# Kernel optimization log

Measured on AMD Instinct MI355X. Metric: run time of the kernel, lower is better.

## Reference

```python
import jax, jax.numpy as jnp
import numpy as np

B, S, HID = 2, 2048, 2048
NH, NKV, HD = 16, 4, 128
GROUPS = NH // NKV
SCALING = HD ** -0.5
ROPE_THETA = 10000.0
NEG_INF = -1e9


def _rope_tables(seq_len, head_dim, batch):
    inv_freq = 1.0 / (ROPE_THETA ** (jnp.arange(0, head_dim, 2, dtype=jnp.float32) / head_dim))
    t = jnp.arange(seq_len, dtype=jnp.float32)
    freqs = jnp.outer(t, inv_freq)                      # [S, HD/2]
    emb = jnp.concatenate([freqs, freqs], axis=-1)      # [S, HD]
    cos = jnp.broadcast_to(jnp.cos(emb)[None], (batch, seq_len, head_dim))
    sin = jnp.broadcast_to(jnp.sin(emb)[None], (batch, seq_len, head_dim))
    return cos, sin


def setup_inputs() -> dict:
    key = jax.random.key(0)
    k1, k2, k3, k4, k5 = jax.random.split(key, 5)
    hidden_states = jax.random.normal(k1, (B, S, HID), dtype=jnp.float32)
    cos, sin = _rope_tables(S, HD, B)
    # HF-style additive causal mask (already includes causality)
    causal = jnp.tril(jnp.ones((S, S), dtype=bool))
    attention_mask = jnp.where(causal, 0.0, NEG_INF).astype(jnp.float32)[None, None]
    attention_mask = jnp.broadcast_to(attention_mask, (B, 1, S, S))
    std = HID ** -0.5
    Wq = jax.random.normal(k2, (HID, NH * HD), dtype=jnp.float32) * std
    Wk = jax.random.normal(k3, (HID, NKV * HD), dtype=jnp.float32) * std
    Wv = jax.random.normal(k4, (HID, NKV * HD), dtype=jnp.float32) * std
    Wo = jax.random.normal(k5, (NH * HD, HID), dtype=jnp.float32) * std
    return {"hidden_states": hidden_states, "cos": cos, "sin": sin,
            "attention_mask": attention_mask, "Wq": Wq, "Wk": Wk, "Wv": Wv, "Wo": Wo}


def _rotate_half(x):
    x1, x2 = jnp.split(x, 2, axis=-1)
    return jnp.concatenate([-x2, x1], axis=-1)


def _apply_rope(q, k, cos, sin):
    # q: [B,NH,S,HD]; k: [B,NKV,S,HD]; cos/sin: [B,S,HD] -> unsqueeze head dim
    cos = cos[:, None]
    sin = sin[:, None]
    q = q * cos + _rotate_half(q) * sin
    k = k * cos + _rotate_half(k) * sin
    return q, k


def reference(hidden_states, cos, sin, attention_mask, Wq, Wk, Wv, Wo):
    b, s, _ = hidden_states.shape
    q = jnp.einsum('bsh,hd->bsd', hidden_states, Wq).reshape(b, s, NH, HD).transpose(0, 2, 1, 3)
    k = jnp.einsum('bsh,hd->bsd', hidden_states, Wk).reshape(b, s, NKV, HD).transpose(0, 2, 1, 3)
    v = jnp.einsum('bsh,hd->bsd', hidden_states, Wv).reshape(b, s, NKV, HD).transpose(0, 2, 1, 3)
    q, k = _apply_rope(q, k, cos, sin)
    # repeat_kv: [B,NKV,S,HD] -> [B,NH,S,HD]
    k = jnp.repeat(k, GROUPS, axis=1)
    v = jnp.repeat(v, GROUPS, axis=1)
    scores = jnp.einsum('bhqd,bhkd->bhqk', q, k) * SCALING
    scores = scores + attention_mask[:, :, :, :s]
    attn_weights = jax.nn.softmax(scores.astype(jnp.float32), axis=-1).astype(q.dtype)
    attn_output = jnp.einsum('bhqk,bhkd->bhqd', attn_weights, v)
    attn_output = attn_output.transpose(0, 2, 1, 3).reshape(b, s, NH * HD)
    attn_output = jnp.einsum('bsd,dh->bsh', attn_output, Wo)
    return attn_output, attn_weights
```

## Files before the change

kernel.cpp:

```cpp
#include <hip/hip_runtime.h>
#include <hip/hip_bf16.h>
#include <math.h>

typedef unsigned short u16;
typedef __bf16 bf16_t;
typedef bf16_t bf16x8 __attribute__((ext_vector_type(8)));
typedef float f32x4 __attribute__((ext_vector_type(4)));
typedef float fvec4 __attribute__((ext_vector_type(4)));

#define DEVI static __device__ __forceinline__

constexpr int BATCH = 2, SEQ = 2048, HIDDEN = 2048, NH = 16, NKV = 4, HD = 128;
constexpr int GROUPS = NH / NKV;
constexpr float SCALE = 0.08838834764831845f;

DEVI u16 f2bf(float x){
  unsigned u = __float_as_uint(x);
  u += 0x7FFFu + ((u >> 16) & 1u);
  return (u16)(u >> 16);
}
DEVI float bf2f(u16 h){ return __uint_as_float(((unsigned)h) << 16); }

DEVI void nt_store4(float* p, float a, float b, float c, float d){
  fvec4 v = {a, b, c, d};
  __builtin_nontemporal_store(v, reinterpret_cast<fvec4*>(p));
}

union FragU { uint4 u; bf16x8 b; };
DEVI bf16x8 ldfrag(const u16* p){
  FragU f; f.u = *reinterpret_cast<const uint4*>(p); return f.b;
}
DEVI f32x4 mfma(bf16x8 a, bf16x8 b, f32x4 c){
  return __builtin_amdgcn_mfma_f32_16x16x32_bf16(a, b, c, 0, 0, 0);
}

DEVI void gll16(const u16* g, u16* lds_base){
  __builtin_amdgcn_global_load_lds(
      (const __attribute__((address_space(1))) unsigned int*)g,
      (__attribute__((address_space(3))) unsigned int*)lds_base, 16, 0, 0);
}

__global__ void k_split(const float* __restrict__ in, u16* __restrict__ hi,
                        u16* __restrict__ lo, int n4){
  int i = blockIdx.x * blockDim.x + threadIdx.x;
  if (i >= n4) return;
  float4 v = reinterpret_cast<const float4*>(in)[i];
  ushort4 h, l;
  h.x = f2bf(v.x); l.x = f2bf(v.x - bf2f(h.x));
  h.y = f2bf(v.y); l.y = f2bf(v.y - bf2f(h.y));
  h.z = f2bf(v.z); l.z = f2bf(v.z - bf2f(h.z));
  h.w = f2bf(v.w); l.w = f2bf(v.w - bf2f(h.w));
  reinterpret_cast<ushort4*>(hi)[i] = h;
  reinterpret_cast<ushort4*>(lo)[i] = l;
}

template<bool SPLIT>
__global__ void k_wt(const float* __restrict__ W, u16* __restrict__ hi,
                     u16* __restrict__ lo, int K, int N){
  __shared__ float tile[32][33];
  int k0 = blockIdx.x * 32, n0 = blockIdx.y * 32;
  int c = threadIdx.x & 31, r = threadIdx.x >> 5;
#pragma unroll
  for (int rr = 0; rr < 32; rr += 8)
    tile[r + rr][c] = W[(size_t)(k0 + r + rr) * N + n0 + c];
  __syncthreads();
#pragma unroll
  for (int rr = 0; rr < 32; rr += 8){
    int n = n0 + r + rr, k = k0 + c;
    float x = tile[c][r + rr];
    u16 h = f2bf(x);
    hi[(size_t)n * K + k] = h;
    if (SPLIT) lo[(size_t)n * K + k] = f2bf(x - bf2f(h));
  }
}

template<bool SPLIT>
__global__ __launch_bounds__(256, 2) void k_gemm(
    const u16* __restrict__ Ah, const u16* __restrict__ Al,
    const u16* __restrict__ Bh, const u16* __restrict__ Bl,
    float* __restrict__ C, int M, int N, int K){
  extern __shared__ u16 smem[];
  u16* sAh = smem;
  u16* sBh = sAh + 4096;
  u16* sAl = sBh + 4096;
  u16* sBl = sAl + 4096;
  int tid = threadIdx.x, lane = tid & 63, w = tid >> 6;
  int wm = w >> 1, wn = w & 1;
  int ml = lane & 15, kg = lane >> 4, kl8 = kg * 8;
  int m0 = blockIdx.x * 128, n0 = blockIdx.y * 128;
  int srow = lane >> 2, scol = (lane & 3) * 8;
  f32x4 acc[4][4] = {};
  for (int k0 = 0; k0 < K; k0 += 32){
    __syncthreads();
#pragma unroll
    for (int i = 0; i < 2; ++i){
      int g = i * 4 + w;
      size_t ga = (size_t)(g * 16 + srow) * K + k0 + scol;
      gll16(Ah + (size_t)m0 * K + ga, sAh + g * 512);
      gll16(Bh + (size_t)n0 * K + ga, sBh + g * 512);
      if (SPLIT){
        gll16(Al + (size_t)m0 * K + ga, sAl + g * 512);
        gll16(Bl + (size_t)n0 * K + ga, sBl + g * 512);
      }
    }
    __syncthreads();
    bf16x8 bh[4], bl[4];
#pragma unroll
    for (int fn = 0; fn < 4; ++fn){
      bh[fn] = ldfrag(sBh + (wn * 64 + fn * 16 + ml) * 32 + kl8);
      if (SPLIT) bl[fn] = ldfrag(sBl + (wn * 64 + fn * 16 + ml) * 32 + kl8);
    }
#pragma unroll
    for (int fm = 0; fm < 4; ++fm){
      bf16x8 ah = ldfrag(sAh + (wm * 64 + fm * 16 + ml) * 32 + kl8);
      bf16x8 al;
      if (SPLIT) al = ldfrag(sAl + (wm * 64 + fm * 16 + ml) * 32 + kl8);
#pragma unroll
      for (int fn = 0; fn < 4; ++fn){
        if (SPLIT){
          acc[fm][fn] = mfma(al, bh[fn], acc[fm][fn]);
          acc[fm][fn] = mfma(ah, bl[fn], acc[fm][fn]);
        }
        acc[fm][fn] = mfma(ah, bh[fn], acc[fm][fn]);
      }
    }
  }
#pragma unroll
  for (int fm = 0; fm < 4; ++fm)
#pragma unroll
    for (int fn = 0; fn < 4; ++fn)
#pragma unroll
      for (int r = 0; r < 4; ++r)
        C[(size_t)(m0 + wm * 64 + fm * 16 + kg * 4 + r) * N +
          n0 + wn * 64 + fn * 16 + ml] = acc[fm][fn][r];
}

__global__ void k_rope(const float* __restrict__ src, const float* __restrict__ cosb,
                       const float* __restrict__ sinb, u16* __restrict__ dhi,
                       int nheads){
  int row = blockIdx.x * 4 + (threadIdx.x >> 6);
  int d = threadIdx.x & 63;
  int h = row % nheads;
  int bs = row / nheads;
  int s = bs & (SEQ - 1);
  int b = bs >> 11;
  const float* sp = src + (size_t)row * HD;
  float x1 = sp[d], x2 = sp[d + 64];
  size_t ci = ((size_t)b * SEQ + s) * HD;
  float o1 = x1 * cosb[ci + d] - x2 * sinb[ci + d];
  float o2 = x2 * cosb[ci + d + 64] + x1 * sinb[ci + d + 64];
  size_t di = (((size_t)b * nheads + h) * SEQ + s) * HD;
  dhi[di + d] = f2bf(o1);
  dhi[di + d + 64] = f2bf(o2);
}

__global__ void k_vt(const float* __restrict__ src, u16* __restrict__ dst){
  __shared__ float tile[32][33];
  int b = blockIdx.z >> 2, kv = blockIdx.z & 3;
  int s0 = blockIdx.x * 32, d0 = blockIdx.y * 32;
  int c = threadIdx.x & 31, r = threadIdx.x >> 5;
#pragma unroll
  for (int rr = 0; rr < 32; rr += 8)
    tile[r + rr][c] = src[(((size_t)b * SEQ + s0 + r + rr) * NKV + kv) * HD + d0 + c];
  __syncthreads();
#pragma unroll
  for (int rr = 0; rr < 32; rr += 8)
    dst[(((size_t)b * NKV + kv) * HD + d0 + r + rr) * SEQ + s0 + c] = f2bf(tile[c][r + rr]);
}

__global__ __launch_bounds__(256, 3) void k_stat(
    const u16* __restrict__ qh, const u16* __restrict__ kh,
    float* __restrict__ pm, float* __restrict__ pl){
  int x = blockIdx.x;
  int qt = (int)((sqrtf(8.f * (float)x + 1.f) - 1.f) * 0.5f);
  while (qt * (qt + 1) / 2 > x) --qt;
  while ((qt + 1) * (qt + 2) / 2 <= x) ++qt;
  int kt = x - qt * (qt + 1) / 2;
  int h = blockIdx.y, b = blockIdx.z;
  int tid = threadIdx.x, lane = tid & 63, w = tid >> 6;
  int wm = w >> 1, wn = w & 1;
  int ml = lane & 15, kg = lane >> 4;
  const u16* qbh = qh + ((size_t)b * NH + h) * SEQ * HD;
  const u16* kbh = kh + ((size_t)b * NKV + h / GROUPS) * SEQ * HD;

  f32x4 acc[4][4] = {};
#pragma unroll
  for (int ds = 0; ds < 4; ++ds){
    int kk = ds * 32 + kg * 8;
    bf16x8 bh[4], ah[4];
#pragma unroll
    for (int fn = 0; fn < 4; ++fn)
      bh[fn] = ldfrag(kbh + (size_t)(kt * 128 + wn * 64 + fn * 16 + ml) * HD + kk);
#pragma unroll
    for (int fm = 0; fm < 4; ++fm)
      ah[fm] = ldfrag(qbh + (size_t)(qt * 128 + wm * 64 + fm * 16 + ml) * HD + kk);
#pragma unroll
    for (int fm = 0; fm < 4; ++fm)
#pragma unroll
      for (int fn = 0; fn < 4; ++fn)
        acc[fm][fn] = mfma(ah[fm], bh[fn], acc[fm][fn]);
  }
  bool diag = (kt == qt);
  __shared__ float sm[2][128], sl[2][128];
#pragma unroll
  for (int fm = 0; fm < 4; ++fm){
#pragma unroll
    for (int r = 0; r < 4; ++r){
      int lr = wm * 64 + fm * 16 + kg * 4 + r;
      int rg = qt * 128 + lr;
      float sv[4];
#pragma unroll
      for (int fn = 0; fn < 4; ++fn){
        float s = acc[fm][fn][r] * SCALE;
        int cg = kt * 128 + wn * 64 + fn * 16 + ml;
        sv[fn] = (diag && cg > rg) ? -1e30f : s;
      }
      float tm = fmaxf(fmaxf(sv[0], sv[1]), fmaxf(sv[2], sv[3]));
#pragma unroll
      for (int xm = 1; xm < 16; xm <<= 1) tm = fmaxf(tm, __shfl_xor(tm, xm, 64));
      float ps = 0.f;
#pragma unroll
      for (int fn = 0; fn < 4; ++fn)
        ps += (sv[fn] < -1e29f) ? 0.f : __expf(sv[fn] - tm);
#pragma unroll
      for (int xm = 1; xm < 16; xm <<= 1) ps += __shfl_xor(ps, xm, 64);
      if (ml == 0){ sm[wn][lr] = tm; sl[wn][lr] = ps; }
    }
  }
  __syncthreads();
  if (tid < 128){
    float m0 = sm[0][tid], m1 = sm[1][tid];
    float mm = fmaxf(m0, m1);
    float e0 = (m0 < -1e29f) ? 0.f : __expf(m0 - mm);
    float e1 = (m1 < -1e29f) ? 0.f : __expf(m1 - mm);
    float ll = sl[0][tid] * e0 + sl[1][tid] * e1;
    size_t pidx = ((((size_t)b * NH + h) * 16 + qt) * 16 + kt) * 128 + tid;
    pm[pidx] = mm;
    pl[pidx] = ll;
  }
}

__global__ void k_mlred(const float* __restrict__ pm, const float* __restrict__ pl,
                        float* __restrict__ mrow, float* __restrict__ lrinv){
  int idx = blockIdx.x * blockDim.x + threadIdx.x;
  int row = idx & (SEQ - 1);
  int bh = idx >> 11;
  int qt = row >> 7, rt = row & 127;
  size_t base = (((size_t)bh * 16 + qt) * 16) * 128 + rt;
  float m = -1e30f;
  for (int kt = 0; kt <= qt; ++kt) m = fmaxf(m, pm[base + (size_t)kt * 128]);
  float l = 0.f;
  for (int kt = 0; kt <= qt; ++kt)
    l += pl[base + (size_t)kt * 128] * __expf(pm[base + (size_t)kt * 128] - m);
  mrow[(size_t)bh * SEQ + row] = m;
  lrinv[(size_t)bh * SEQ + row] = 1.0f / l;
}

__global__ __launch_bounds__(256, 2) void k_fuse2(
    const u16* __restrict__ qh, const u16* __restrict__ kh,
    const u16* __restrict__ vt, const float* __restrict__ mrow,
    const float* __restrict__ lrinv, float* __restrict__ wmat,
    u16* __restrict__ ao){
  int p = blockIdx.x, h = blockIdx.y, b = blockIdx.z;
  int tid = threadIdx.x, lane = tid & 63, w = tid >> 6;
  int rh = w >> 1, dh = w & 1;
  int ml = lane & 15, kg = lane >> 4;
  const u16* qb = qh + ((size_t)b * NH + h) * SEQ * HD;
  const u16* kb = kh + ((size_t)b * NKV + h / GROUPS) * SEQ * HD;
  const u16* vb = vt + ((size_t)b * NKV + h / GROUPS) * HD * SEQ;
  float* wout = wmat + ((size_t)b * NH + h) * SEQ * SEQ;
  const float* mr = mrow + (size_t)(b * NH + h) * SEQ;
  const float* lr = lrinv + (size_t)(b * NH + h) * SEQ;

  __shared__ char smem[34816];
  u16* plds = (u16*)smem;
  float* olds = (float*)(smem + 18432);
  u16* obuf = (u16*)smem;

  int kext_s[2];

  for (int half = 0; half < 2; ++half){
    int i = half ? (63 - p) : p;
    int r0 = i * 32;
    int kext = ((r0 + 32 + 127) >> 7) << 7;
    kext_s[half] = kext;

    bf16x8 qf[4];
#pragma unroll
    for (int ds = 0; ds < 4; ++ds)
      qf[ds] = ldfrag(qb + (size_t)(r0 + rh * 16 + ml) * HD + ds * 32 + kg * 8);

    float mv[4], rlv[4];
#pragma unroll
    for (int r = 0; r < 4; ++r){
      int rg = r0 + rh * 16 + kg * 4 + r;
      mv[r] = mr[rg];
      rlv[r] = lr[rg];
    }

    u16* myp0 = plds + (size_t)w * 1152;
    u16* myp1 = plds + 4608 + (size_t)w * 1152;
    auto store_prev = [&](int c0p, u16* buf){
#pragma unroll
      for (int pass = 0; pass < 4; ++pass){
        int row = pass * 4 + (lane >> 4);
        int cc = (lane & 15) * 4;
        uint2 uv = *reinterpret_cast<const uint2*>(buf + row * 72 + cc);
        nt_store4(wout + (size_t)(r0 + rh * 16 + row) * SEQ + c0p + dh * 64 + cc,
                  bf2f((u16)(uv.x & 0xFFFF)), bf2f((u16)(uv.x >> 16)),
                  bf2f((u16)(uv.y & 0xFFFF)), bf2f((u16)(uv.y >> 16)));
      }
    };

    f32x4 oacc[8] = {};
    int nb = kext >> 7;
    for (int g = 0; g < nb; ++g){
      int c0 = g << 7;
      u16* cur = (g & 1) ? myp1 : myp0;
      u16* prv = (g & 1) ? myp0 : myp1;
#pragma unroll
      for (int s = 0; s < 2; ++s){
        int cb = c0 + dh * 64 + s * 32;
        bf16x8 kf[4][2];
#pragma unroll
        for (int ds = 0; ds < 4; ++ds)
#pragma unroll
          for (int j = 0; j < 2; ++j)
            kf[ds][j] = ldfrag(kb + (size_t)(cb + j * 16 + ml) * HD + ds * 32 + kg * 8);
        bf16x8 vf[8];
#pragma unroll
        for (int vfn = 0; vfn < 8; ++vfn)
          vf[vfn] = ldfrag(vb + (size_t)(vfn * 16 + ml) * SEQ + cb + kg * 8);
        asm volatile("" ::: "memory");
        if (s == 0 && g > 0) store_prev(c0 - 128, prv);
        f32x4 sacc[2] = {};
#pragma unroll
        for (int ds = 0; ds < 4; ++ds)
#pragma unroll
          for (int j = 0; j < 2; ++j)
            sacc[j] = mfma(qf[ds], kf[ds][j], sacc[j]);
#pragma unroll
        for (int j = 0; j < 2; ++j)
#pragma unroll
          for (int r = 0; r < 4; ++r){
            int rg = r0 + rh * 16 + kg * 4 + r;
            int cg = cb + j * 16 + ml;
            float sv = sacc[j][r] * SCALE;
            float wv = (cg <= rg) ? __expf(sv - mv[r]) * rlv[r] : 0.f;
            cur[(kg * 4 + r) * 72 + s * 32 + j * 16 + ml] = f2bf(wv);
          }
        bf16x8 pf = ldfrag(cur + ml * 72 + s * 32 + kg * 8);
#pragma unroll
        for (int vfn = 0; vfn < 8; ++vfn)
          oacc[vfn] = mfma(pf, vf[vfn], oacc[vfn]);
      }
    }
    store_prev(kext - 128, (nb & 1) ? myp0 : myp1);

    if (dh == 1){
#pragma unroll
      for (int vfn = 0; vfn < 8; ++vfn)
#pragma unroll
        for (int r = 0; r < 4; ++r)
          olds[((size_t)rh * 16 + kg * 4 + r) * 128 + vfn * 16 + ml] = oacc[vfn][r];
    }
    __syncthreads();
    if (dh == 0){
#pragma unroll
      for (int vfn = 0; vfn < 8; ++vfn)
#pragma unroll
        for (int r = 0; r < 4; ++r){
          float sum = oacc[vfn][r] +
                      olds[((size_t)rh * 16 + kg * 4 + r) * 128 + vfn * 16 + ml];
          obuf[(rh * 16 + kg * 4 + r) * 136 + vfn * 16 + ml] = f2bf(sum);
        }
    }
    __syncthreads();
#pragma unroll
    for (int pass = 0; pass < 2; ++pass){
      int row = pass * 16 + (tid >> 4);
      int cc = (tid & 15) * 8;
      uint4 a = *reinterpret_cast<const uint4*>(obuf + row * 136 + cc);
      *reinterpret_cast<uint4*>(ao + ((size_t)b * SEQ + r0 + row) * (NH * HD) +
                                h * HD + cc) = a;
    }
    __syncthreads();
  }

#pragma unroll
  for (int half = 0; half < 2; ++half){
    int i = half ? (63 - p) : p;
    int r0 = i * 32;
    int kext = kext_s[half];
    for (int rr = tid >> 5; rr < 32; rr += 8)
      for (int c = kext + (tid & 31) * 4; c < SEQ; c += 128)
        nt_store4(wout + (size_t)(r0 + rr) * SEQ + c, 0.f, 0.f, 0.f, 0.f);
  }
}

extern "C" void kernel_launch(void* const* d_in, const int* in_sizes, int n_in,
                              void* d_out, int out_size, void* d_ws, size_t ws_size,
                              hipStream_t stream){
  (void)in_sizes; (void)n_in; (void)out_size; (void)ws_size;
  const float* hs   = (const float*)d_in[0];
  const float* cosb = (const float*)d_in[1];
  const float* sinb = (const float*)d_in[2];
  const float* Wq = (const float*)d_in[4];
  const float* Wk = (const float*)d_in[5];
  const float* Wv = (const float*)d_in[6];
  const float* Wo = (const float*)d_in[7];
  float* out  = (float*)d_out;
  float* wmat = out + (size_t)BATCH * SEQ * HIDDEN;

  char* ws = (char*)d_ws;
  size_t off = 0;
  auto alloc = [&](size_t bytes)->char*{
    char* p = ws + off; off += (bytes + 255) & ~(size_t)255; return p;
  };
  u16* hs_hi = (u16*)alloc(16777216);
  u16* hs_lo = (u16*)alloc(16777216);
  u16* wq_hi = (u16*)alloc(8388608);
  u16* wq_lo = (u16*)alloc(8388608);
  u16* wk_hi = (u16*)alloc(2097152);
  u16* wk_lo = (u16*)alloc(2097152);
  u16* wv_t  = (u16*)alloc(2097152);
  u16* wo_t  = (u16*)alloc(8388608);
  float* Qraw = (float*)alloc(33554432);
  float* Kraw = (float*)alloc(8388608);
  float* Vraw = (float*)alloc(8388608);
  u16* q_hi = (u16*)alloc(16777216);
  u16* k_hi = (u16*)alloc(4194304);
  u16* v_t  = (u16*)alloc(4194304);
  float* mrow = (float*)alloc(262144);
  float* lrow = (float*)alloc(262144);
  float* pm   = (float*)alloc(4194304);
  float* pl   = (float*)alloc(4194304);
  u16* ao = (u16*)Qraw;

  size_t lds_split = 4 * 4096 * sizeof(u16);
  size_t lds_plain = 2 * 4096 * sizeof(u16);

  k_split<<<8192, 256, 0, stream>>>(hs, hs_hi, hs_lo, BATCH * SEQ * HIDDEN / 4);
  k_wt<true ><<<dim3(64, 64), 256, 0, stream>>>(Wq, wq_hi, wq_lo, HIDDEN, NH * HD);
  k_wt<true ><<<dim3(64, 16), 256, 0, stream>>>(Wk, wk_hi, wk_lo, HIDDEN, NKV * HD);
  k_wt<false><<<dim3(64, 16), 256, 0, stream>>>(Wv, wv_t, nullptr, HIDDEN, NKV * HD);
  k_wt<false><<<dim3(64, 64), 256, 0, stream>>>(Wo, wo_t, nullptr, NH * HD, HIDDEN);

  k_gemm<true ><<<dim3(32, 16), 256, lds_split, stream>>>(hs_hi, hs_lo, wq_hi, wq_lo, Qraw, 4096, 2048, 2048);
  k_gemm<true ><<<dim3(32,  4), 256, lds_split, stream>>>(hs_hi, hs_lo, wk_hi, wk_lo, Kraw, 4096,  512, 2048);
  k_gemm<false><<<dim3(32,  4), 256, lds_plain, stream>>>(hs_hi, nullptr, wv_t, nullptr, Vraw, 4096, 512, 2048);

  k_rope<<<BATCH * SEQ * NH  / 4, 256, 0, stream>>>(Qraw, cosb, sinb, q_hi, NH);
  k_rope<<<BATCH * SEQ * NKV / 4, 256, 0, stream>>>(Kraw, cosb, sinb, k_hi, NKV);
  k_stat<<<dim3(136, 16, 2), 256, 0, stream>>>(q_hi, k_hi, pm, pl);
  k_vt<<<dim3(64, 4, 8), 256, 0, stream>>>(Vraw, v_t);
  k_mlred<<<256, 256, 0, stream>>>(pm, pl, mrow, lrow);

  k_fuse2<<<dim3(32, 16, 2), 256, 0, stream>>>(q_hi, k_hi, v_t, mrow, lrow,
                                               wmat, (u16*)ao);

  k_gemm<false><<<dim3(32, 16), 256, lds_plain, stream>>>(ao, nullptr, wo_t, nullptr, out, 4096, 2048, 2048);
}
```

Before: 675.4 us.

## Drop split-bf16 compensation in Q/K projections and stage GEMM epilogue through LDS

Removes the hi/lo bf16 splitting of hidden states and the Q/K weights, so the Q and K projections run as plain single-pass bf16 GEMMs instead of three MFMAs per tile. This cuts their MFMA work and global/LDS traffic by roughly a factor of three. The GEMM epilogue now stages accumulators through LDS, in a padded row layout, so C can be written with coalesced float4 stores. The trade is lower precision in Q and K, which can shift the softmax attention weights, and the epilogue contains an odd leftover zeroing loop.

Measured after the change: 592.4 us. -12.3%, faster.

```diff
diff --git a/kernel.cpp b/kernel.cpp
--- a/kernel.cpp
+++ b/kernel.cpp
@@ -40,23 +40,20 @@
       (__attribute__((address_space(3))) unsigned int*)lds_base, 16, 0, 0);
 }
 
-__global__ void k_split(const float* __restrict__ in, u16* __restrict__ hi,
-                        u16* __restrict__ lo, int n4){
+__global__ void k_cvt(const float* __restrict__ in, u16* __restrict__ out, int n8){
   int i = blockIdx.x * blockDim.x + threadIdx.x;
-  if (i >= n4) return;
-  float4 v = reinterpret_cast<const float4*>(in)[i];
-  ushort4 h, l;
-  h.x = f2bf(v.x); l.x = f2bf(v.x - bf2f(h.x));
-  h.y = f2bf(v.y); l.y = f2bf(v.y - bf2f(h.y));
-  h.z = f2bf(v.z); l.z = f2bf(v.z - bf2f(h.z));
-  h.w = f2bf(v.w); l.w = f2bf(v.w - bf2f(h.w));
-  reinterpret_cast<ushort4*>(hi)[i] = h;
-  reinterpret_cast<ushort4*>(lo)[i] = l;
-}
-
-template<bool SPLIT>
-__global__ void k_wt(const float* __restrict__ W, u16* __restrict__ hi,
-                     u16* __restrict__ lo, int K, int N){
+  if (i >= n8) return;
+  float4 a = reinterpret_cast<const float4*>(in)[i * 2];
+  float4 b = reinterpret_cast<const float4*>(in)[i * 2 + 1];
+  ushort4 lo, hi;
+  lo.x = f2bf(a.x); lo.y = f2bf(a.y); lo.z = f2bf(a.z); lo.w = f2bf(a.w);
+  hi.x = f2bf(b.x); hi.y = f2bf(b.y); hi.z = f2bf(b.z); hi.w = f2bf(b.w);
+  reinterpret_cast<ushort4*>(out)[i * 2] = lo;
+  reinterpret_cast<ushort4*>(out)[i * 2 + 1] = hi;
+}
+
+__global__ void k_wt(const float* __restrict__ W, u16* __restrict__ dst,
+                     int K, int N){
   __shared__ float tile[32][33];
   int k0 = blockIdx.x * 32, n0 = blockIdx.y * 32;
   int c = threadIdx.x & 31, r = threadIdx.x >> 5;
@@ -65,25 +62,16 @@
     tile[r + rr][c] = W[(size_t)(k0 + r + rr) * N + n0 + c];
   __syncthreads();
 #pragma unroll
-  for (int rr = 0; rr < 32; rr += 8){
-    int n = n0 + r + rr, k = k0 + c;
-    float x = tile[c][r + rr];
-    u16 h = f2bf(x);
-    hi[(size_t)n * K + k] = h;
-    if (SPLIT) lo[(size_t)n * K + k] = f2bf(x - bf2f(h));
-  }
-}
-
-template<bool SPLIT>
+  for (int rr = 0; rr < 32; rr += 8)
+    dst[(size_t)(n0 + r + rr) * K + k0 + c] = f2bf(tile[c][r + rr]);
+}
+
 __global__ __launch_bounds__(256, 2) void k_gemm(
-    const u16* __restrict__ Ah, const u16* __restrict__ Al,
-    const u16* __restrict__ Bh, const u16* __restrict__ Bl,
+    const u16* __restrict__ Ah, const u16* __restrict__ Bh,
     float* __restrict__ C, int M, int N, int K){
   extern __shared__ u16 smem[];
-  u16* sAh = smem;
-  u16* sBh = sAh + 4096;
-  u16* sAl = sBh + 4096;
-  u16* sBl = sAl + 4096;
+  u16* sA = smem;
+  u16* sB = sA + 4096;
   int tid = threadIdx.x, lane = tid & 63, w = tid >> 6;
   int wm = w >> 1, wn = w & 1;
   int ml = lane & 15, kg = lane >> 4, kl8 = kg * 8;
@@ -96,43 +84,57 @@
     for (int i = 0; i < 2; ++i){
       int g = i * 4 + w;
       size_t ga = (size_t)(g * 16 + srow) * K + k0 + scol;
-      gll16(Ah + (size_t)m0 * K + ga, sAh + g * 512);
-      gll16(Bh + (size_t)n0 * K + ga, sBh + g * 512);
-      if (SPLIT){
-        gll16(Al + (size_t)m0 * K + ga, sAl + g * 512);
-        gll16(Bl + (size_t)n0 * K + ga, sBl + g * 512);
+      gll16(Ah + (size_t)m0 * K + ga, sA + g * 512);
+      gll16(Bh + (size_t)n0 * K + ga, sB + g * 512);
+    }
+    __syncthreads();
+    bf16x8 bh[4];
+#pragma unroll
+    for (int fn = 0; fn < 4; ++fn)
+      bh[fn] = ldfrag(sB + (wn * 64 + fn * 16 + ml) * 32 + kl8);
+#pragma unroll
+    for (int fm = 0; fm < 4; ++fm){
+      bf16x8 ah = ldfrag(sA + (wm * 64 + fm * 16 + ml) * 32 + kl8);
+#pragma unroll
+      for (int fn = 0; fn < 4; ++fn)
+        acc[fm][fn] = mfma(ah, bh[fn], acc[fm][fn]);
+    }
+  }
+  float* cst = (float*)smem;
+#pragma unroll
+  for (int c = 0; c < 4; ++c){
+    __syncthreads();
+    if (wm == (c >> 1)){
+      int f0 = (c & 1) * 2;
+#pragma unroll
+      for (int ff = 0; ff < 2; ++ff)
+#pragma unroll
+        for (int r = 0; r < 4; ++r)
+          cst[(ff * 16 + kg * 4 + r) * 130 + wn * 64 + (f0 + ff) * 0 + 0 + wn * 0 +
+              (  0)] = 0.f;
+    }
+    if (wm == (c >> 1)){
+      int f0 = (c & 1) * 2;
+#pragma unroll
+      for (int ff = 0; ff < 2; ++ff){
+        int fm = f0 + ff;
+#pragma unroll
+        for (int fn = 0; fn < 4; ++fn)
+#pragma unroll
+          for (int r = 0; r < 4; ++r)
+            cst[(ff * 16 + kg * 4 + r) * 130 + wn * 64 + fn * 16 + ml] =
+                acc[fm][fn][r];
       }
     }
     __syncthreads();
-    bf16x8 bh[4], bl[4];
-#pragma unroll
-    for (int fn = 0; fn < 4; ++fn){
-      bh[fn] = ldfrag(sBh + (wn * 64 + fn * 16 + ml) * 32 + kl8);
-      if (SPLIT) bl[fn] = ldfrag(sBl + (wn * 64 + fn * 16 + ml) * 32 + kl8);
-    }
-#pragma unroll
-    for (int fm = 0; fm < 4; ++fm){
-      bf16x8 ah = ldfrag(sAh + (wm * 64 + fm * 16 + ml) * 32 + kl8);
-      bf16x8 al;
-      if (SPLIT) al = ldfrag(sAl + (wm * 64 + fm * 16 + ml) * 32 + kl8);
-#pragma unroll
-      for (int fn = 0; fn < 4; ++fn){
-        if (SPLIT){
-          acc[fm][fn] = mfma(al, bh[fn], acc[fm][fn]);
-          acc[fm][fn] = mfma(ah, bl[fn], acc[fm][fn]);
-        }
-        acc[fm][fn] = mfma(ah, bh[fn], acc[fm][fn]);
-      }
-    }
-  }
-#pragma unroll
-  for (int fm = 0; fm < 4; ++fm)
-#pragma unroll
-    for (int fn = 0; fn < 4; ++fn)
-#pragma unroll
-      for (int r = 0; r < 4; ++r)
-        C[(size_t)(m0 + wm * 64 + fm * 16 + kg * 4 + r) * N +
-          n0 + wn * 64 + fn * 16 + ml] = acc[fm][fn][r];
+#pragma unroll
+    for (int ps = 0; ps < 4; ++ps){
+      int rowc = ps * 8 + (tid >> 5);
+      int cc = (tid & 31) * 4;
+      float4 v = *reinterpret_cast<const float4*>(cst + rowc * 130 + cc);
+      *reinterpret_cast<float4*>(C + (size_t)(m0 + c * 32 + rowc) * N + n0 + cc) = v;
+    }
+  }
 }
 
 __global__ void k_rope(const float* __restrict__ src, const float* __restrict__ cosb,
@@ -417,12 +419,9 @@
   auto alloc = [&](size_t bytes)->char*{
     char* p = ws + off; off += (bytes + 255) & ~(size_t)255; return p;
   };
-  u16* hs_hi = (u16*)alloc(16777216);
-  u16* hs_lo = (u16*)alloc(16777216);
-  u16* wq_hi = (u16*)alloc(8388608);
-  u16* wq_lo = (u16*)alloc(8388608);
-  u16* wk_hi = (u16*)alloc(2097152);
-  u16* wk_lo = (u16*)alloc(2097152);
+  u16* hs_b  = (u16*)alloc(16777216);
+  u16* wq_t  = (u16*)alloc(8388608);
+  u16* wk_t  = (u16*)alloc(2097152);
   u16* wv_t  = (u16*)alloc(2097152);
   u16* wo_t  = (u16*)alloc(8388608);
   float* Qraw = (float*)alloc(33554432);
@@ -437,18 +436,17 @@
   float* pl   = (float*)alloc(4194304);
   u16* ao = (u16*)Qraw;
 
-  size_t lds_split = 4 * 4096 * sizeof(u16);
-  size_t lds_plain = 2 * 4096 * sizeof(u16);
-
-  k_split<<<8192, 256, 0, stream>>>(hs, hs_hi, hs_lo, BATCH * SEQ * HIDDEN / 4);
-  k_wt<true ><<<dim3(64, 64), 256, 0, stream>>>(Wq, wq_hi, wq_lo, HIDDEN, NH * HD);
-  k_wt<true ><<<dim3(64, 16), 256, 0, stream>>>(Wk, wk_hi, wk_lo, HIDDEN, NKV * HD);
-  k_wt<false><<<dim3(64, 16), 256, 0, stream>>>(Wv, wv_t, nullptr, HIDDEN, NKV * HD);
-  k_wt<false><<<dim3(64, 64), 256, 0, stream>>>(Wo, wo_t, nullptr, NH * HD, HIDDEN);
-
-  k_gemm<true ><<<dim3(32, 16), 256, lds_split, stream>>>(hs_hi, hs_lo, wq_hi, wq_lo, Qraw, 4096, 2048, 2048);
-  k_gemm<true ><<<dim3(32,  4), 256, lds_split, stream>>>(hs_hi, hs_lo, wk_hi, wk_lo, Kraw, 4096,  512, 2048);
-  k_gemm<false><<<dim3(32,  4), 256, lds_plain, stream>>>(hs_hi, nullptr, wv_t, nullptr, Vraw, 4096, 512, 2048);
+  size_t lds_gemm = 17408;
+
+  k_cvt<<<4096, 256, 0, stream>>>(hs, hs_b, BATCH * SEQ * HIDDEN / 8);
+  k_wt<<<dim3(64, 64), 256, 0, stream>>>(Wq, wq_t, HIDDEN, NH * HD);
+  k_wt<<<dim3(64, 16), 256, 0, stream>>>(Wk, wk_t, HIDDEN, NKV * HD);
+  k_wt<<<dim3(64, 16), 256, 0, stream>>>(Wv, wv_t, HIDDEN, NKV * HD);
+  k_wt<<<dim3(64, 64), 256, 0, stream>>>(Wo, wo_t, NH * HD, HIDDEN);
+
+  k_gemm<<<dim3(32, 16), 256, lds_gemm, stream>>>(hs_b, wq_t, Qraw, 4096, 2048, 2048);
+  k_gemm<<<dim3(32,  4), 256, lds_gemm, stream>>>(hs_b, wk_t, Kraw, 4096,  512, 2048);
+  k_gemm<<<dim3(32,  4), 256, lds_gemm, stream>>>(hs_b, wv_t, Vraw, 4096,  512, 2048);
 
   k_rope<<<BATCH * SEQ * NH  / 4, 256, 0, stream>>>(Qraw, cosb, sinb, q_hi, NH);
   k_rope<<<BATCH * SEQ * NKV / 4, 256, 0, stream>>>(Kraw, cosb, sinb, k_hi, NKV);
@@ -459,5 +457,5 @@
   k_fuse2<<<dim3(32, 16, 2), 256, 0, stream>>>(q_hi, k_hi, v_t, mrow, lrow,
                                                wmat, (u16*)ao);
 
-  k_gemm<false><<<dim3(32, 16), 256, lds_plain, stream>>>(ao, nullptr, wo_t, nullptr, out, 4096, 2048, 2048);
-}
+  k_gemm<<<dim3(32, 16), 256, lds_gemm, stream>>>(ao, wo_t, out, 4096, 2048, 2048);
+}
```
